# Kernel optimization log

Hardware: AMD Instinct MI355X
Metric: run time of the kernel (lower is better)

Reference implementation:

```python
import jax, jax.numpy as jnp
import numpy as np


def setup_inputs() -> dict:
    key = jax.random.key(0)
    k1, k2, k3 = jax.random.split(key, 3)
    B, inCh, H, W = 16, 64, 128, 128
    outCh, sub, kh, kw = 128, 8, 3, 3
    # match torch uniform init bound: k = 1/(sub*kh*kw)
    bound = (1.0 / (sub * kh * kw)) ** 0.5
    X = jax.random.normal(k1, (B, inCh, H, W), dtype=jnp.float32)
    weights = jax.random.uniform(k2, (outCh, 1, sub, kh, kw), dtype=jnp.float32, minval=-bound, maxval=bound)
    biases = jax.random.uniform(k3, (outCh, 1), dtype=jnp.float32, minval=-bound, maxval=bound)
    return {"X": X, "weights": weights, "biases": biases}


def reference(X, weights, biases):
    # X: [B, inCh, H, W]; weights: [outCh, 1, sub, kh, kw]; biases: [outCh, 1]
    B, inCh, H, W = X.shape
    outCh, _, sub, kh, kw = weights.shape
    # valid-conv output size (module adds +1 only for odd kernels; kh=kw=3 odd)
    h = H - kh + (1 if kh % 2 != 0 else 0)
    w = W - kw + (1 if kw % 2 != 0 else 0)
    # channel tiling: repeated channel c == original channel c % inCh
    desired = outCh + sub - 1
    idx = jnp.arange(desired) % inCh
    Xr = X[:, idx]                      # [B, desired, H, W]
    Wsq = weights[:, 0]                 # [outCh, sub, kh, kw]
    # out[b,o,y,x] = sum_{s,i,j} Xr[b, o+s, y+i, x+j] * W[o,s,i,j]
    # = sum over s of a depthwise (groups=outCh) valid conv on channel slice [s:s+outCh]
    out = jnp.zeros((B, outCh, h, w), dtype=X.dtype)
    for s in range(sub):
        xs = jax.lax.slice_in_dim(Xr, s, s + outCh, axis=1)   # [B, outCh, H, W]
        ws = Wsq[:, s][:, None]                               # [outCh, 1, kh, kw] (OIHW)
        out = out + jax.lax.conv_general_dilated(
            xs, ws, window_strides=(1, 1), padding="VALID",
            feature_group_count=outCh)
    out = out + biases[:, 0][None, :, None, None]
    return out
```

## Files before the change

### kernel.cpp

```cpp
#include <hip/hip_runtime.h>

#define BATCH 16
#define INCH  64
#define IMH   128
#define IMW   128
#define OUTCH 128
#define SUB   8
#define OH    126
#define OW    126

#define YT 8
#define XT 16
#define TR (YT + 2)
#define RS 20
#define CHS (TR * RS)

__global__ __launch_bounds__(256, 3)
void Group_Conv_84731114815961_kernel(const float* __restrict__ X,
                                      const float* __restrict__ Wg,
                                      const float* __restrict__ Bias,
                                      float* __restrict__ Out) {
    __shared__ float xin[INCH * CHS];

    const int tx  = blockIdx.x;
    const int ty  = blockIdx.y;
    const int b   = blockIdx.z;
    const int x0  = tx * XT;
    const int y0  = ty * YT;
    const int tid = threadIdx.x;

    const float* Xb = X + (size_t)b * INCH * IMH * IMW;
    #pragma unroll
    for (int it = 0; it < (INCH * CHS / 4 + 255) / 256; ++it) {
        int k = tid + it * 256;
        if (k < INCH * CHS / 4) {
            int fi  = k * 4;
            int c   = fi / CHS;
            int rem = fi - c * CHS;
            int r   = rem / RS;
            int col = rem - r * RS;
            int sr = y0 + r;  if (sr > IMH - 1) sr = IMH - 1;
            int sc = x0 + col; if (sc > IMW - 4) sc = IMW - 4;
            const float4 v = *reinterpret_cast<const float4*>(Xb + (c * IMH + sr) * IMW + sc);
            *reinterpret_cast<float4*>(&xin[fi]) = v;
        }
    }
    __syncthreads();

    const int p  = tid >> 2;
    const int xg = tid & 3;
    const int cb = xg * 4;

    float acc0[YT][4];
    float acc1[YT][4];
    #pragma unroll
    for (int y = 0; y < YT; ++y)
        #pragma unroll
        for (int q = 0; q < 4; ++q) { acc0[y][q] = 0.f; acc1[y][q] = 0.f; }

    for (int s = 0; s < SUB; ++s) {
        const int c = (p + s) & 63;
        const float* w0p = Wg + (p * SUB + s) * 9;
        const float* w1p = Wg + ((p + 64) * SUB + s) * 9;
        float w0[9], w1[9];
        #pragma unroll
        for (int t = 0; t < 9; ++t) { w0[t] = w0p[t]; w1[t] = w1p[t]; }

        const float* base = &xin[c * CHS + cb];
        #pragma unroll
        for (int r = 0; r < TR; ++r) {
            float v[6];
            const float4 a  = *reinterpret_cast<const float4*>(base + r * RS);
            const float2 b2 = *reinterpret_cast<const float2*>(base + r * RS + 4);
            v[0] = a.x; v[1] = a.y; v[2] = a.z; v[3] = a.w; v[4] = b2.x; v[5] = b2.y;
            #pragma unroll
            for (int i = 0; i < 3; ++i) {
                const int yo = r - i;
                if (yo >= 0 && yo < YT) {
                    #pragma unroll
                    for (int j = 0; j < 3; ++j) {
                        const float ww0 = w0[i * 3 + j];
                        const float ww1 = w1[i * 3 + j];
                        #pragma unroll
                        for (int q = 0; q < 4; ++q) {
                            acc0[yo][q] = fmaf(v[q + j], ww0, acc0[yo][q]);
                            acc1[yo][q] = fmaf(v[q + j], ww1, acc1[yo][q]);
                        }
                    }
                }
            }
        }
    }

    const float bz0 = Bias[p];
    const float bz1 = Bias[p + 64];
    const int   xcol = x0 + cb;
    float* O0 = Out + (((size_t)b * OUTCH + p)      * OH) * OW;
    float* O1 = Out + (((size_t)b * OUTCH + p + 64) * OH) * OW;

    #pragma unroll
    for (int y = 0; y < YT; ++y) {
        const int oy = y0 + y;
        if (oy < OH) {
            float* o0 = O0 + oy * OW + xcol;
            float* o1 = O1 + oy * OW + xcol;
            if (xcol + 3 < OW) {
                float4 s0, s1;
                s0.x = acc0[y][0] + bz0; s0.y = acc0[y][1] + bz0;
                s0.z = acc0[y][2] + bz0; s0.w = acc0[y][3] + bz0;
                s1.x = acc1[y][0] + bz1; s1.y = acc1[y][1] + bz1;
                s1.z = acc1[y][2] + bz1; s1.w = acc1[y][3] + bz1;
                *reinterpret_cast<float4*>(o0) = s0;
                *reinterpret_cast<float4*>(o1) = s1;
            } else {
                #pragma unroll
                for (int q = 0; q < 4; ++q) {
                    if (xcol + q < OW) {
                        o0[q] = acc0[y][q] + bz0;
                        o1[q] = acc1[y][q] + bz1;
                    }
                }
            }
        }
    }
}

extern "C" void kernel_launch(void* const* d_in, const int* in_sizes, int n_in,
                              void* d_out, int out_size, void* d_ws, size_t ws_size,
                              hipStream_t stream) {
    const float* X    = (const float*)d_in[0];
    const float* Wg   = (const float*)d_in[1];
    const float* Bias = (const float*)d_in[2];
    float*       Out  = (float*)d_out;

    dim3 grid(8, 16, 16);
    Group_Conv_84731114815961_kernel<<<grid, 256, 0, stream>>>(X, Wg, Bias, Out);
}
```

Baseline: 102.1 us.

## Halve row tile, use direct global-to-LDS loads, repack weights, remap blocks

Cuts the output row tile from 8 to 4 and raises the occupancy hint, so more smaller blocks run per CU. The shared-memory fill now uses the global_load_lds builtin, which writes straight into LDS without a register round trip. A small prep kernel repacks the weights into 80-byte-aligned per-channel chunks so each thread loads them as float4 vectors. A 1D grid with a swizzled block index changes the order tiles are scheduled across XCDs. The trade-off is more halo overhead per output row and an extra kernel launch.

```diff
diff --git a/kernel.cpp b/kernel.cpp
--- a/kernel.cpp
+++ b/kernel.cpp
@@ -9,47 +9,68 @@
 #define OH    126
 #define OW    126
 
-#define YT 8
+#define YT 4
 #define XT 16
 #define TR (YT + 2)
 #define RS 20
 #define CHS (TR * RS)
+#define LDS_FLOATS (INCH * CHS)
+#define LDS_VEC4   (LDS_FLOATS / 4)
 
-__global__ __launch_bounds__(256, 3)
+#define GLOAD_LDS(g, l) __builtin_amdgcn_global_load_lds( \
+    (const __attribute__((address_space(1))) void*)(g),   \
+    (__attribute__((address_space(3))) void*)(l), 16, 0, 0)
+
+__global__ __launch_bounds__(256)
+void prep_weights_kernel(const float* __restrict__ Wg, float* __restrict__ Wp) {
+    int idx = blockIdx.x * 256 + threadIdx.x;
+    if (idx < 512 * 18) {
+        int chunk = idx / 18;
+        int t     = idx - chunk * 18;
+        int s = chunk >> 6;
+        int p = chunk & 63;
+        int o  = (t < 9) ? p : p + 64;
+        int tt = (t < 9) ? t : t - 9;
+        Wp[chunk * 20 + t] = Wg[(o * SUB + s) * 9 + tt];
+    }
+}
+
+__global__ __launch_bounds__(256, 5)
 void Group_Conv_84731114815961_kernel(const float* __restrict__ X,
                                       const float* __restrict__ Wg,
                                       const float* __restrict__ Bias,
+                                      const float* __restrict__ Wp,
                                       float* __restrict__ Out) {
-    __shared__ float xin[INCH * CHS];
+    __shared__ float xin[LDS_FLOATS];
 
-    const int tx  = blockIdx.x;
-    const int ty  = blockIdx.y;
-    const int b   = blockIdx.z;
+    const int bid = blockIdx.x;
+    const int wg  = (bid & 7) * 512 + (bid >> 3);
+    const int tx  = wg & 7;
+    const int ty  = (wg >> 3) & 31;
+    const int b   = wg >> 8;
     const int x0  = tx * XT;
     const int y0  = ty * YT;
     const int tid = threadIdx.x;
 
     const float* Xb = X + (size_t)b * INCH * IMH * IMW;
     #pragma unroll
-    for (int it = 0; it < (INCH * CHS / 4 + 255) / 256; ++it) {
-        int k = tid + it * 256;
-        if (k < INCH * CHS / 4) {
-            int fi  = k * 4;
-            int c   = fi / CHS;
-            int rem = fi - c * CHS;
-            int r   = rem / RS;
-            int col = rem - r * RS;
-            int sr = y0 + r;  if (sr > IMH - 1) sr = IMH - 1;
+    for (int it = 0; it < 8; ++it) {
+        int k = it * 256 + tid;
+        if (k < LDS_VEC4) {
+            int c   = k / 30;
+            int rem = k - c * 30;
+            int r   = rem / 5;
+            int col = (rem - r * 5) * 4;
+            int sr = y0 + r;   if (sr > IMH - 1) sr = IMH - 1;
             int sc = x0 + col; if (sc > IMW - 4) sc = IMW - 4;
-            const float4 v = *reinterpret_cast<const float4*>(Xb + (c * IMH + sr) * IMW + sc);
-            *reinterpret_cast<float4*>(&xin[fi]) = v;
+            GLOAD_LDS(Xb + (c * IMH + sr) * IMW + sc, &xin[k * 4]);
         }
     }
     __syncthreads();
 
     const int p  = tid >> 2;
     const int xg = tid & 3;
-    const int cb = xg * 4;
+    const int cb = xg << 2;
 
     float acc0[YT][4];
     float acc1[YT][4];
@@ -58,20 +79,33 @@
         #pragma unroll
         for (int q = 0; q < 4; ++q) { acc0[y][q] = 0.f; acc1[y][q] = 0.f; }
 
+    const bool useWp = (Wp != nullptr);
+
     for (int s = 0; s < SUB; ++s) {
         const int c = (p + s) & 63;
-        const float* w0p = Wg + (p * SUB + s) * 9;
-        const float* w1p = Wg + ((p + 64) * SUB + s) * 9;
         float w0[9], w1[9];
-        #pragma unroll
-        for (int t = 0; t < 9; ++t) { w0[t] = w0p[t]; w1[t] = w1p[t]; }
+        if (useWp) {
+            const float4* wc = reinterpret_cast<const float4*>(Wp + ((s << 6) + p) * 20);
+            const float4 f0 = wc[0], f1 = wc[1], f2 = wc[2], f3 = wc[3], f4 = wc[4];
+            w0[0]=f0.x; w0[1]=f0.y; w0[2]=f0.z; w0[3]=f0.w;
+            w0[4]=f1.x; w0[5]=f1.y; w0[6]=f1.z; w0[7]=f1.w;
+            w0[8]=f2.x;
+            w1[0]=f2.y; w1[1]=f2.z; w1[2]=f2.w;
+            w1[3]=f3.x; w1[4]=f3.y; w1[5]=f3.z; w1[6]=f3.w;
+            w1[7]=f4.x; w1[8]=f4.y;
+        } else {
+            const float* w0p = Wg + (p * SUB + s) * 9;
+            const float* w1p = Wg + ((p + 64) * SUB + s) * 9;
+            #pragma unroll
+            for (int t = 0; t < 9; ++t) { w0[t] = w0p[t]; w1[t] = w1p[t]; }
+        }
 
         const float* base = &xin[c * CHS + cb];
         #pragma unroll
         for (int r = 0; r < TR; ++r) {
-            float v[6];
             const float4 a  = *reinterpret_cast<const float4*>(base + r * RS);
             const float2 b2 = *reinterpret_cast<const float2*>(base + r * RS + 4);
+            float v[6];
             v[0] = a.x; v[1] = a.y; v[2] = a.z; v[3] = a.w; v[4] = b2.x; v[5] = b2.y;
             #pragma unroll
             for (int i = 0; i < 3; ++i) {
@@ -133,6 +167,11 @@
     const float* Bias = (const float*)d_in[2];
     float*       Out  = (float*)d_out;
 
-    dim3 grid(8, 16, 16);
-    Group_Conv_84731114815961_kernel<<<grid, 256, 0, stream>>>(X, Wg, Bias, Out);
+    float* Wp = nullptr;
+    if (d_ws && ws_size >= 512 * 20 * sizeof(float)) {
+        Wp = (float*)d_ws;
+        prep_weights_kernel<<<36, 256, 0, stream>>>(Wg, Wp);
+    }
+
+    Group_Conv_84731114815961_kernel<<<4096, 256, 0, stream>>>(X, Wg, Bias, Wp, Out);
 }
```

Result: slower. 239.1 us (+134.1%).
